# Optimization experiments

Hardware: AMD Instinct MI355X
Metric: run time of the kernel (lower is better)

## Reference

```python
import jax, jax.numpy as jnp
import numpy as np
from jax import lax

IN_CH = 192
CENTER_CH = 192
MID_CH = 192
K = 3
BS, H, W = 8, 64, 64
MASK_NUM = 16


def conv2d(x, w, b, padding=0, groups=1):
    # x: (N,C,H,W), w: (O, I/groups, kh, kw)
    out = lax.conv_general_dilated(
        x, w, window_strides=(1, 1),
        padding=[(padding, padding), (padding, padding)],
        dimension_numbers=('NCHW', 'OIHW', 'NCHW'),
        feature_group_count=groups)
    return out + b[None, :, None, None]


def lrelu(x):
    return jax.nn.leaky_relu(x, negative_slope=0.1)


def setup_inputs() -> dict:
    key = jax.random.key(0)
    ks = jax.random.split(key, 32)
    s = 0.02
    d = {
        'input': jax.random.normal(ks[0], (BS, IN_CH, H, W), jnp.float32),
        'list_center': jax.random.normal(ks[1], (BS, MASK_NUM, CENTER_CH), jnp.float32),
        'batch_mask': jax.random.randint(ks[2], (BS, H, W), 0, MASK_NUM),
        # self.conv: conv1x1(in,mid) -> lrelu -> conv1x1(mid,mid)
        'w0': jax.random.normal(ks[3], (MID_CH, IN_CH, 1, 1)) * s,
        'b0': jnp.zeros((MID_CH,)),
        'w1': jax.random.normal(ks[4], (MID_CH, MID_CH, 1, 1)) * s,
        'b1': jnp.zeros((MID_CH,)),
        # k_sp_gen: conv1x1(mid+center,mid), 3x3(mid,mid), depthwise 3x3(mid -> mid*k^2, groups=mid)
        'ws0': jax.random.normal(ks[5], (MID_CH, MID_CH + CENTER_CH, 1, 1)) * s,
        'bs0': jnp.zeros((MID_CH,)),
        'ws1': jax.random.normal(ks[6], (MID_CH, MID_CH, K, K)) * s,
        'bs1': jnp.zeros((MID_CH,)),
        'ws2': jax.random.normal(ks[7], (MID_CH * K * K, 1, K, K)) * s,
        'bs2': jnp.zeros((MID_CH * K * K,)),
        # k_ch_gen: GAP -> conv1x1 -> lrelu -> conv1x1 -> sigmoid
        'wc0': jax.random.normal(ks[8], (MID_CH, MID_CH, 1, 1)) * s,
        'bc0': jnp.zeros((MID_CH,)),
        'wc1': jax.random.normal(ks[9], (MID_CH, MID_CH, 1, 1)) * s,
        'bc1': jnp.zeros((MID_CH,)),
        # conv_out
        'wo': jax.random.normal(ks[10], (IN_CH, MID_CH, 1, 1)) * s,
        'bo': jnp.zeros((IN_CH,)),
    }
    return d


def mask_expand(list_center, batch_mask):
    # list_center: (bs, mask_num, ch); batch_mask: (bs, h, w) int
    # -> (bs, ch, h, w)
    gathered = jax.vmap(lambda c, m: c[m])(list_center, batch_mask)  # (bs,h,w,ch)
    return jnp.transpose(gathered, (0, 3, 1, 2))


def dynamic_conv(x, k_sp, k):
    # x: (bs, ch, h, w); k_sp: (bs, ch, k^2, h, w)
    bs, ch, h, w = x.shape
    p = (k - 1) // 2
    xp = jnp.pad(x, ((0, 0), (0, 0), (p, p), (p, p)))
    # torch Unfold ordering: kernel index = ki*k + kj, channel-major in view
    patches = jnp.stack([xp[:, :, i:i + h, j:j + w]
                         for i in range(k) for j in range(k)], axis=2)
    return jnp.einsum('bckhw,bckhw->bchw', patches, k_sp)


def reference(input, list_center, batch_mask, w0, b0, w1, b1, ws0, bs0,
              ws1, bs1, ws2, bs2, wc0, bc0, wc1, bc1, wo, bo):
    bs, _, h, w = input.shape
    k = K
    ch = MID_CH
    centers_exp = mask_expand(list_center, batch_mask)  # (bs, center_ch, h, w)
    shortcut = input
    x = conv2d(lrelu(conv2d(input, w0, b0)), w1, b1)  # self.conv
    y = jnp.concatenate([x, centers_exp], axis=1)
    y = lrelu(conv2d(y, ws0, bs0))
    y = lrelu(conv2d(y, ws1, bs1, padding=(k - 1) // 2))
    k_sp = conv2d(y, ws2, bs2, padding=(k - 1) // 2, groups=ch)
    k_sp = k_sp.reshape(bs, ch, k * k, h, w)
    out = dynamic_conv(x, k_sp, k)
    # squeeze-excite channel gate
    g = jnp.mean(out, axis=(2, 3), keepdims=True)
    g = jax.nn.sigmoid(conv2d(lrelu(conv2d(g, wc0, bc0)), wc1, bc1))
    out = g * out
    out = conv2d(out, wo, bo)
    return out + shortcut
```

## Files before the change

### kernel.cpp

```cpp
#include <hip/hip_runtime.h>
#include <hip/hip_bf16.h>

#define CH   192
#define PIX  4096
#define BSZ  8

using f32x4  = __attribute__((ext_vector_type(4))) float;
using short8 = __attribute__((ext_vector_type(8))) short;

__device__ __forceinline__ float bf2f(unsigned short u) {
    union { unsigned u32; float f; } x; x.u32 = ((unsigned)u) << 16; return x.f;
}
__device__ __forceinline__ unsigned short f2bf(float f) {
    union { float f; unsigned u; } x; x.f = f;
    unsigned u = x.u;
    unsigned r = (u + 0x7FFFu + ((u >> 16) & 1u)) >> 16;
    return (unsigned short)r;
}

__device__ __forceinline__ short8 ldsB(const unsigned short* Bsm, int k0, int px) {
    short8 f;
    #pragma unroll
    for (int e = 0; e < 8; ++e) f[e] = (short)Bsm[(k0 + e) * 66 + px];
    return f;
}

__global__ void k_cvt_in(const float* __restrict__ in, unsigned short* __restrict__ out) {
    int i = blockIdx.x * 256 + threadIdx.x;
    float4 v = ((const float4*)in)[i];
    ushort4 o;
    o.x = f2bf(v.x); o.y = f2bf(v.y); o.z = f2bf(v.z); o.w = f2bf(v.w);
    ((ushort4*)out)[i] = o;
}

__global__ void k_prep_w(const float* __restrict__ w0, const float* __restrict__ w1,
                         const float* __restrict__ ws0, const float* __restrict__ wo,
                         const float* __restrict__ ws1,
                         unsigned short* __restrict__ w0f, unsigned short* __restrict__ w1f,
                         unsigned short* __restrict__ ws0xf, unsigned short* __restrict__ wof,
                         unsigned short* __restrict__ wc3f, float* __restrict__ gsum) {
    int i = blockIdx.x * 256 + threadIdx.x;
    if (i < 4*36864) {
        int which = i / 36864, j = i % 36864;
        int kc = j / 6144, r = j % 6144, mf = r / 512, r2 = r % 512;
        int l = r2 >> 3, e = r2 & 7;
        int o = mf*16 + (l & 15), k = kc*32 + ((l >> 4) << 3) + e;
        float v;
        unsigned short* dst;
        if (which == 0)      { v = w0[o*192 + k];  dst = w0f;   }
        else if (which == 1) { v = w1[o*192 + k];  dst = w1f;   }
        else if (which == 2) { v = ws0[o*384 + k]; dst = ws0xf; }
        else                 { v = wo[o*192 + k];  dst = wof;   }
        dst[j] = f2bf(v);
        return;
    }
    i -= 4*36864;
    if (i < 331776) {
        int tk = i / 6144, tap = tk / 6, kc = tk % 6;
        int r = i % 6144, mf = r / 512, r2 = r % 512;
        int l = r2 >> 3, e = r2 & 7;
        int o = mf*16 + (l & 15), c = kc*32 + ((l >> 4) << 3) + e;
        wc3f[i] = f2bf(ws1[(o*192 + c)*9 + tap]);
        return;
    }
    i -= 331776;
    if (i < 1536) gsum[i] = 0.f;
}

__global__ void k_tcent(const float* __restrict__ ws0, const float* __restrict__ lc,
                        float* __restrict__ tc) {
    int m = blockIdx.x, b = blockIdx.y, o = threadIdx.x;
    __shared__ float cbuf[192];
    cbuf[o] = lc[(b*16 + m)*192 + o];
    __syncthreads();
    float a = 0.f;
    const float* wr = ws0 + o*384 + 192;
    for (int c = 0; c < 192; ++c) a += wr[c] * cbuf[c];
    tc[(b*16 + m)*192 + o] = a;
}

__global__ __launch_bounds__(256) void k_fused3(
    const unsigned short* __restrict__ inb,
    const unsigned short* __restrict__ w0f,
    const unsigned short* __restrict__ w1f,
    const unsigned short* __restrict__ ws0xf,
    const float* __restrict__ b0, const float* __restrict__ b1,
    const float* __restrict__ bs0,
    const float* __restrict__ tc, const int* __restrict__ mask,
    unsigned short* __restrict__ xg, unsigned short* __restrict__ y0g)
{
    const int b = blockIdx.y, n0 = blockIdx.x * 64;
    __shared__ unsigned short Bsm[192*66];
    __shared__ unsigned short Csm[192*66];
    const int tid = threadIdx.x, lane = tid & 63, wv = tid >> 6;
    const int li = lane & 15, kq = lane >> 4;

    {
        const unsigned short* src = inb + (size_t)b*192*PIX + n0;
        #pragma unroll
        for (int j = 0; j < 6; ++j) {
            int q = tid + 256*j, k = q >> 3, g = q & 7;
            uint4 v = *(const uint4*)(src + (size_t)k*PIX + g*8);
            unsigned* d = (unsigned*)(Bsm + k*66 + g*8);
            const unsigned* s = (const unsigned*)&v;
            d[0]=s[0]; d[1]=s[1]; d[2]=s[2]; d[3]=s[3];
        }
    }
    __syncthreads();

    f32x4 acc[3][4];

    #pragma unroll
    for (int m = 0; m < 3; ++m)
        #pragma unroll
        for (int n = 0; n < 4; ++n) acc[m][n] = {0.f,0.f,0.f,0.f};
    for (int kc = 0; kc < 6; ++kc) {
        short8 a[3];
        #pragma unroll
        for (int m = 0; m < 3; ++m)
            a[m] = *(const short8*)(w0f + ((kc*12 + wv*3 + m)*64 + lane)*8);
        #pragma unroll
        for (int n = 0; n < 4; ++n) {
            short8 fb = ldsB(Bsm, kc*32 + kq*8, n*16 + li);
            #pragma unroll
            for (int m = 0; m < 3; ++m)
                acc[m][n] = __builtin_amdgcn_mfma_f32_16x16x32_bf16(a[m], fb, acc[m][n], 0,0,0);
        }
    }
    #pragma unroll
    for (int m = 0; m < 3; ++m) {
        int o0 = (wv*3 + m)*16 + kq*4;
        #pragma unroll
        for (int n = 0; n < 4; ++n) {
            int px = n*16 + li;
            #pragma unroll
            for (int r = 0; r < 4; ++r) {
                float v = acc[m][n][r] + b0[o0 + r];
                v = v > 0.f ? v : 0.1f*v;
                Csm[(o0 + r)*66 + px] = f2bf(v);
            }
        }
    }
    __syncthreads();

    #pragma unroll
    for (int m = 0; m < 3; ++m)
        #pragma unroll
        for (int n = 0; n < 4; ++n) acc[m][n] = {0.f,0.f,0.f,0.f};
    for (int kc = 0; kc < 6; ++kc) {
        short8 a[3];
        #pragma unroll
        for (int m = 0; m < 3; ++m)
            a[m] = *(const short8*)(w1f + ((kc*12 + wv*3 + m)*64 + lane)*8);
        #pragma unroll
        for (int n = 0; n < 4; ++n) {
            short8 fb = ldsB(Csm, kc*32 + kq*8, n*16 + li);
            #pragma unroll
            for (int m = 0; m < 3; ++m)
                acc[m][n] = __builtin_amdgcn_mfma_f32_16x16x32_bf16(a[m], fb, acc[m][n], 0,0,0);
        }
    }
    #pragma unroll
    for (int m = 0; m < 3; ++m) {
        int o0 = (wv*3 + m)*16 + kq*4;
        #pragma unroll
        for (int n = 0; n < 4; ++n) {
            int px = n*16 + li;
            #pragma unroll
            for (int r = 0; r < 4; ++r) {
                float v = acc[m][n][r] + b1[o0 + r];
                unsigned short h = f2bf(v);
                Bsm[(o0 + r)*66 + px] = h;
                xg[((size_t)b*192 + o0 + r)*PIX + n0 + px] = h;
            }
        }
    }
    __syncthreads();

    #pragma unroll
    for (int m = 0; m < 3; ++m)
        #pragma unroll
        for (int n = 0; n < 4; ++n) acc[m][n] = {0.f,0.f,0.f,0.f};
    for (int kc = 0; kc < 6; ++kc) {
        short8 a[3];
        #pragma unroll
        for (int m = 0; m < 3; ++m)
            a[m] = *(const short8*)(ws0xf + ((kc*12 + wv*3 + m)*64 + lane)*8);
        #pragma unroll
        for (int n = 0; n < 4; ++n) {
            short8 fb = ldsB(Bsm, kc*32 + kq*8, n*16 + li);
            #pragma unroll
            for (int m = 0; m < 3; ++m)
                acc[m][n] = __builtin_amdgcn_mfma_f32_16x16x32_bf16(a[m], fb, acc[m][n], 0,0,0);
        }
    }
    int mi_[4];
    #pragma unroll
    for (int n = 0; n < 4; ++n) mi_[n] = mask[b*PIX + n0 + n*16 + li];
    #pragma unroll
    for (int m = 0; m < 3; ++m) {
        int o0 = (wv*3 + m)*16 + kq*4;
        #pragma unroll
        for (int n = 0; n < 4; ++n) {
            int px = n*16 + li;
            const float* tcb = tc + (b*16 + mi_[n])*192;
            #pragma unroll
            for (int r = 0; r < 4; ++r) {
                float v = acc[m][n][r] + bs0[o0 + r] + tcb[o0 + r];
                v = v > 0.f ? v : 0.1f*v;
                y0g[((size_t)b*192 + o0 + r)*PIX + n0 + px] = f2bf(v);
            }
        }
    }
}

__global__ __launch_bounds__(256) void k_conv3n(
    const unsigned short* __restrict__ wc3f,
    const unsigned short* __restrict__ y0,
    const float* __restrict__ bias,
    unsigned short* __restrict__ y1)
{
    const int b = blockIdx.y, h = blockIdx.x;
    __shared__ unsigned short Bs[3*32*66];
    const int tid = threadIdx.x, lane = tid & 63, wv = tid >> 6;
    const int li = lane & 15, kq = lane >> 4;

    f32x4 acc[3][4];
    #pragma unroll
    for (int m = 0; m < 3; ++m)
        #pragma unroll
        for (int n = 0; n < 4; ++n) acc[m][n] = {0.f,0.f,0.f,0.f};

    if (tid < 96) Bs[tid*66] = 0;
    else if (tid < 192) Bs[(tid-96)*66 + 65] = 0;

    for (int kc = 0; kc < 6; ++kc) {
        #pragma unroll
        for (int j = 0; j < 3; ++j) {
            int q = tid*3 + j;
            int dr = q >> 8, k = (q >> 3) & 31, w8 = (q & 7)*8;
            int hh = h + dr - 1;
            uint4 v = {0u,0u,0u,0u};
            if (hh >= 0 && hh < 64)
                v = *(const uint4*)(y0 + ((size_t)b*192 + kc*32 + k)*PIX + hh*64 + w8);
            const unsigned short* pv = (const unsigned short*)&v;
            unsigned short* dst = Bs + (dr*32 + k)*66 + 1 + w8;
            #pragma unroll
            for (int e = 0; e < 8; ++e) dst[e] = pv[e];
        }
        __syncthreads();

        #pragma unroll
        for (int tap = 0; tap < 9; ++tap) {
            const int dr = tap / 3, dc1 = tap % 3;
            short8 a[3];
            #pragma unroll
            for (int m = 0; m < 3; ++m)
                a[m] = *(const short8*)(wc3f + (((tap*6 + kc)*12 + wv*3 + m)*64 + lane)*8);
            #pragma unroll
            for (int n = 0; n < 4; ++n) {
                short8 fb = ldsB(Bs + dr*32*66, kq*8, n*16 + li + dc1);
                #pragma unroll
                for (int m = 0; m < 3; ++m)
                    acc[m][n] = __builtin_amdgcn_mfma_f32_16x16x32_bf16(a[m], fb, acc[m][n], 0,0,0);
            }
        }
        __syncthreads();
    }

    #pragma unroll
    for (int m = 0; m < 3; ++m) {
        int o0 = (wv*3 + m)*16 + kq*4;
        #pragma unroll
        for (int n = 0; n < 4; ++n) {
            int px = h*64 + n*16 + li;
            #pragma unroll
            for (int r = 0; r < 4; ++r) {
                float v = acc[m][n][r] + bias[o0 + r];
                v = v > 0.f ? v : 0.1f*v;
                y1[((size_t)b*192 + o0 + r)*PIX + px] = f2bf(v);
            }
        }
    }
}

__global__ __launch_bounds__(256) void k_dwdyn2(
    const unsigned short* __restrict__ Y1,
    const unsigned short* __restrict__ X,
    const float* __restrict__ ws2,
    const float* __restrict__ bs2,
    unsigned short* __restrict__ OP,
    float* __restrict__ gsum)
{
    const int c = blockIdx.x, b = blockIdx.y;
    __shared__ unsigned short ysm[4096];
    __shared__ unsigned short xsm[4096];
    __shared__ float wsm[81], bsm9[9], red[4];
    const int tid = threadIdx.x;
    const size_t cb = ((size_t)b*192 + c) * PIX;
    #pragma unroll
    for (int j = 0; j < 2; ++j) {
        int i = tid + 256*j;
        *(uint4*)(ysm + i*8) = *(const uint4*)(Y1 + cb + i*8);
        *(uint4*)(xsm + i*8) = *(const uint4*)(X  + cb + i*8);
    }
    if (tid < 81) wsm[tid] = ws2[c*81 + tid];
    else if (tid < 90) bsm9[tid-81] = bs2[c*9 + tid - 81];
    __syncthreads();

    float gacc = 0.f;
    for (int i = 0; i < 16; ++i) {
        int px = tid + 256*i, hh = px >> 6, ww = px & 63;
        float ksp[9];
        #pragma unroll
        for (int j = 0; j < 9; ++j) ksp[j] = bsm9[j];
        #pragma unroll
        for (int tap = 0; tap < 9; ++tap) {
            int h2 = hh + tap/3 - 1, w2 = ww + tap%3 - 1;
            float yv = ((unsigned)h2 < 64u && (unsigned)w2 < 64u)
                       ? bf2f(ysm[h2*64 + w2]) : 0.f;
            #pragma unroll
            for (int j = 0; j < 9; ++j) ksp[j] += yv * wsm[j*9 + tap];
        }
        float out = 0.f;
        #pragma unroll
        for (int j = 0; j < 9; ++j) {
            int h2 = hh + j/3 - 1, w2 = ww + j%3 - 1;
            float xv = ((unsigned)h2 < 64u && (unsigned)w2 < 64u)
                       ? bf2f(xsm[h2*64 + w2]) : 0.f;
            out += xv * ksp[j];
        }
        OP[cb + px] = f2bf(out);
        gacc += out;
    }
    #pragma unroll
    for (int off = 32; off > 0; off >>= 1) gacc += __shfl_down(gacc, off);
    if ((tid & 63) == 0) red[tid >> 6] = gacc;
    __syncthreads();
    if (tid == 0) gsum[b*192 + c] = red[0] + red[1] + red[2] + red[3];
}

__global__ void k_gate(const float* __restrict__ gsum,
                       const float* __restrict__ wc0, const float* __restrict__ bc0,
                       const float* __restrict__ wc1, const float* __restrict__ bc1,
                       float* __restrict__ gvec)
{
    const int b = blockIdx.x, t = threadIdx.x;
    __shared__ float mean[192], s1[192];
    mean[t] = gsum[b*192 + t] * (1.f/4096.f);
    __syncthreads();
    float a = bc0[t];
    const float* w = wc0 + t*192;
    for (int i = 0; i < 192; ++i) a += w[i] * mean[i];
    s1[t] = a > 0.f ? a : 0.1f * a;
    __syncthreads();
    float a2 = bc1[t];
    const float* w2 = wc1 + t*192;
    for (int i = 0; i < 192; ++i) a2 += w2[i] * s1[i];
    gvec[b*192 + t] = 1.f / (1.f + __expf(-a2));
}

__global__ __launch_bounds__(256) void k_gemmo(
    const unsigned short* __restrict__ wof,
    const unsigned short* __restrict__ op,
    const float* __restrict__ bo,
    const float* __restrict__ gvec,
    const float* __restrict__ resid,
    float* __restrict__ out)
{
    const int b = blockIdx.y, n0 = blockIdx.x * 64;
    __shared__ unsigned short Bsm[192*66];
    const int tid = threadIdx.x, lane = tid & 63, wv = tid >> 6;
    const int li = lane & 15, kq = lane >> 4;

    {
        const unsigned short* src = op + (size_t)b*192*PIX + n0;
        #pragma unroll
        for (int j = 0; j < 6; ++j) {
            int q = tid + 256*j, k = q >> 3, g = q & 7;
            uint4 v = *(const uint4*)(src + (size_t)k*PIX + g*8);
            float gs = gvec[b*192 + k];
            unsigned short* pv = (unsigned short*)&v;
            #pragma unroll
            for (int e = 0; e < 8; ++e) pv[e] = f2bf(bf2f(pv[e]) * gs);
            unsigned* d = (unsigned*)(Bsm + k*66 + g*8);
            const unsigned* s = (const unsigned*)&v;
            d[0]=s[0]; d[1]=s[1]; d[2]=s[2]; d[3]=s[3];
        }
    }
    __syncthreads();

    f32x4 acc[3][4];
    #pragma unroll
    for (int m = 0; m < 3; ++m)
        #pragma unroll
        for (int n = 0; n < 4; ++n) acc[m][n] = {0.f,0.f,0.f,0.f};
    for (int kc = 0; kc < 6; ++kc) {
        short8 a[3];
        #pragma unroll
        for (int m = 0; m < 3; ++m)
            a[m] = *(const short8*)(wof + ((kc*12 + wv*3 + m)*64 + lane)*8);
        #pragma unroll
        for (int n = 0; n < 4; ++n) {
            short8 fb = ldsB(Bsm, kc*32 + kq*8, n*16 + li);
            #pragma unroll
            for (int m = 0; m < 3; ++m)
                acc[m][n] = __builtin_amdgcn_mfma_f32_16x16x32_bf16(a[m], fb, acc[m][n], 0,0,0);
        }
    }
    #pragma unroll
    for (int m = 0; m < 3; ++m) {
        int o0 = (wv*3 + m)*16 + kq*4;
        #pragma unroll
        for (int n = 0; n < 4; ++n) {
            int px = n*16 + li;
            #pragma unroll
            for (int r = 0; r < 4; ++r) {
                size_t idx = ((size_t)b*192 + o0 + r)*PIX + n0 + px;
                out[idx] = acc[m][n][r] + bo[o0 + r] + resid[idx];
            }
        }
    }
}

extern "C" void kernel_launch(void* const* d_in, const int* in_sizes, int n_in,
                              void* d_out, int out_size, void* d_ws, size_t ws_size,
                              hipStream_t stream)
{
    const float* input = (const float*)d_in[0];
    const float* lc    = (const float*)d_in[1];
    const int*   mask  = (const int*)d_in[2];
    const float* w0  = (const float*)d_in[3];
    const float* b0  = (const float*)d_in[4];
    const float* w1  = (const float*)d_in[5];
    const float* b1  = (const float*)d_in[6];
    const float* ws0 = (const float*)d_in[7];
    const float* bs0 = (const float*)d_in[8];
    const float* ws1 = (const float*)d_in[9];
    const float* bs1 = (const float*)d_in[10];
    const float* ws2 = (const float*)d_in[11];
    const float* bs2 = (const float*)d_in[12];
    const float* wc0 = (const float*)d_in[13];
    const float* bc0 = (const float*)d_in[14];
    const float* wc1 = (const float*)d_in[15];
    const float* bc1 = (const float*)d_in[16];
    const float* wo  = (const float*)d_in[17];
    const float* bo  = (const float*)d_in[18];

    char* ws = (char*)d_ws;
    size_t off = 0;
    auto alloc = [&](size_t bytes) {
        void* p = ws + off; off = (off + bytes + 255) & ~(size_t)255; return p;
    };
    const size_t act_b = (size_t)BSZ * CH * PIX * 2;
    unsigned short* in_bf = (unsigned short*)alloc(act_b);
    unsigned short* x_bf  = (unsigned short*)alloc(act_b);
    unsigned short* y0_bf = (unsigned short*)alloc(act_b);
    unsigned short* y1_bf = (unsigned short*)alloc(act_b);
    unsigned short* op_bf = (unsigned short*)alloc(act_b);
    unsigned short* w0f   = (unsigned short*)alloc(36864*2);
    unsigned short* w1f   = (unsigned short*)alloc(36864*2);
    unsigned short* ws0xf = (unsigned short*)alloc(36864*2);
    unsigned short* wof   = (unsigned short*)alloc(36864*2);
    unsigned short* wc3f  = (unsigned short*)alloc(331776*2);
    float* tc   = (float*)alloc(8*16*192*4);
    float* gsum = (float*)alloc(1536*4);
    float* gvec = (float*)alloc(1536*4);

    k_cvt_in<<<6144, 256, 0, stream>>>(input, in_bf);
    k_prep_w<<<1878, 256, 0, stream>>>(w0, w1, ws0, wo, ws1, w0f, w1f, ws0xf, wof, wc3f, gsum);
    k_tcent<<<dim3(16, 8), 192, 0, stream>>>(ws0, lc, tc);

    dim3 gg(64, 8);
    k_fused3<<<gg, 256, 0, stream>>>(in_bf, w0f, w1f, ws0xf, b0, b1, bs0, tc, mask, x_bf, y0_bf);
    k_conv3n<<<gg, 256, 0, stream>>>(wc3f, y0_bf, bs1, y1_bf);
    k_dwdyn2<<<dim3(192, 8), 256, 0, stream>>>(y1_bf, x_bf, ws2, bs2, op_bf, gsum);
    k_gate<<<8, 192, 0, stream>>>(gsum, wc0, bc0, wc1, bc1, gvec);
    k_gemmo<<<gg, 256, 0, stream>>>(wof, op_bf, bo, gvec, input, (float*)d_out);
}
```

Measured before the change: 246.9 us.

## Fuse input bf16 cast into first GEMM and use pixel-major y0 for 3x3 conv

Drops the separate fp32-to-bf16 input conversion kernel: the fused 1x1 GEMM kernel now reads fp32 input and converts it while staging into LDS. The y0 intermediate is written channel-contiguous (pixel-major), going through an LDS transpose, so the 3x3 conv kernel can load 16-byte B fragments straight from LDS instead of gathering 8 scalar shorts. The 3x3 conv moves to 512 threads with the pixel tile split across wave pairs. An extra barrier and a padded Csm stride are added so the new transpose can reuse Csm safely, at the cost of more shared memory.

```diff
diff --git a/kernel.cpp b/kernel.cpp
--- a/kernel.cpp
+++ b/kernel.cpp
@@ -18,19 +18,11 @@
     return (unsigned short)r;
 }
 
-__device__ __forceinline__ short8 ldsB(const unsigned short* Bsm, int k0, int px) {
+__device__ __forceinline__ short8 ldsBs(const unsigned short* B, int ST, int k0, int px) {
     short8 f;
     #pragma unroll
-    for (int e = 0; e < 8; ++e) f[e] = (short)Bsm[(k0 + e) * 66 + px];
+    for (int e = 0; e < 8; ++e) f[e] = (short)B[(k0 + e) * ST + px];
     return f;
-}
-
-__global__ void k_cvt_in(const float* __restrict__ in, unsigned short* __restrict__ out) {
-    int i = blockIdx.x * 256 + threadIdx.x;
-    float4 v = ((const float4*)in)[i];
-    ushort4 o;
-    o.x = f2bf(v.x); o.y = f2bf(v.y); o.z = f2bf(v.z); o.w = f2bf(v.w);
-    ((ushort4*)out)[i] = o;
 }
 
 __global__ void k_prep_w(const float* __restrict__ w0, const float* __restrict__ w1,
@@ -80,30 +72,34 @@
 }
 
 __global__ __launch_bounds__(256) void k_fused3(
-    const unsigned short* __restrict__ inb,
+    const float* __restrict__ input,
     const unsigned short* __restrict__ w0f,
     const unsigned short* __restrict__ w1f,
     const unsigned short* __restrict__ ws0xf,
     const float* __restrict__ b0, const float* __restrict__ b1,
     const float* __restrict__ bs0,
     const float* __restrict__ tc, const int* __restrict__ mask,
-    unsigned short* __restrict__ xg, unsigned short* __restrict__ y0g)
+    unsigned short* __restrict__ xg, unsigned short* __restrict__ y0t)
 {
     const int b = blockIdx.y, n0 = blockIdx.x * 64;
     __shared__ unsigned short Bsm[192*66];
-    __shared__ unsigned short Csm[192*66];
+    __shared__ unsigned short Csm[192*67];
     const int tid = threadIdx.x, lane = tid & 63, wv = tid >> 6;
     const int li = lane & 15, kq = lane >> 4;
 
     {
-        const unsigned short* src = inb + (size_t)b*192*PIX + n0;
+        const float* src = input + (size_t)b*192*PIX + n0;
         #pragma unroll
         for (int j = 0; j < 6; ++j) {
-            int q = tid + 256*j, k = q >> 3, g = q & 7;
-            uint4 v = *(const uint4*)(src + (size_t)k*PIX + g*8);
-            unsigned* d = (unsigned*)(Bsm + k*66 + g*8);
-            const unsigned* s = (const unsigned*)&v;
-            d[0]=s[0]; d[1]=s[1]; d[2]=s[2]; d[3]=s[3];
+            int q = tid + 256*j, k = q >> 3, g = (q & 7)*8;
+            float4 v0 = *(const float4*)(src + (size_t)k*PIX + g);
+            float4 v1 = *(const float4*)(src + (size_t)k*PIX + g + 4);
+            unsigned d0 = f2bf(v0.x) | ((unsigned)f2bf(v0.y) << 16);
+            unsigned d1 = f2bf(v0.z) | ((unsigned)f2bf(v0.w) << 16);
+            unsigned d2 = f2bf(v1.x) | ((unsigned)f2bf(v1.y) << 16);
+            unsigned d3 = f2bf(v1.z) | ((unsigned)f2bf(v1.w) << 16);
+            unsigned* d = (unsigned*)(Bsm + k*66 + g);
+            d[0]=d0; d[1]=d1; d[2]=d2; d[3]=d3;
         }
     }
     __syncthreads();
@@ -121,7 +117,7 @@
             a[m] = *(const short8*)(w0f + ((kc*12 + wv*3 + m)*64 + lane)*8);
         #pragma unroll
         for (int n = 0; n < 4; ++n) {
-            short8 fb = ldsB(Bsm, kc*32 + kq*8, n*16 + li);
+            short8 fb = ldsBs(Bsm, 66, kc*32 + kq*8, n*16 + li);
             #pragma unroll
             for (int m = 0; m < 3; ++m)
                 acc[m][n] = __builtin_amdgcn_mfma_f32_16x16x32_bf16(a[m], fb, acc[m][n], 0,0,0);
@@ -137,7 +133,7 @@
             for (int r = 0; r < 4; ++r) {
                 float v = acc[m][n][r] + b0[o0 + r];
                 v = v > 0.f ? v : 0.1f*v;
-                Csm[(o0 + r)*66 + px] = f2bf(v);
+                Csm[(o0 + r)*67 + px] = f2bf(v);
             }
         }
     }
@@ -154,12 +150,13 @@
             a[m] = *(const short8*)(w1f + ((kc*12 + wv*3 + m)*64 + lane)*8);
         #pragma unroll
         for (int n = 0; n < 4; ++n) {
-            short8 fb = ldsB(Csm, kc*32 + kq*8, n*16 + li);
+            short8 fb = ldsBs(Csm, 67, kc*32 + kq*8, n*16 + li);
             #pragma unroll
             for (int m = 0; m < 3; ++m)
                 acc[m][n] = __builtin_amdgcn_mfma_f32_16x16x32_bf16(a[m], fb, acc[m][n], 0,0,0);
         }
     }
+    __syncthreads();
     #pragma unroll
     for (int m = 0; m < 3; ++m) {
         int o0 = (wv*3 + m)*16 + kq*4;
@@ -188,7 +185,7 @@
             a[m] = *(const short8*)(ws0xf + ((kc*12 + wv*3 + m)*64 + lane)*8);
         #pragma unroll
         for (int n = 0; n < 4; ++n) {
-            short8 fb = ldsB(Bsm, kc*32 + kq*8, n*16 + li);
+            short8 fb = ldsBs(Bsm, 66, kc*32 + kq*8, n*16 + li);
             #pragma unroll
             for (int m = 0; m < 3; ++m)
                 acc[m][n] = __builtin_amdgcn_mfma_f32_16x16x32_bf16(a[m], fb, acc[m][n], 0,0,0);
@@ -204,49 +201,54 @@
         for (int n = 0; n < 4; ++n) {
             int px = n*16 + li;
             const float* tcb = tc + (b*16 + mi_[n])*192;
+            ushort4 w;
+            unsigned short* wp = (unsigned short*)&w;
             #pragma unroll
             for (int r = 0; r < 4; ++r) {
                 float v = acc[m][n][r] + bs0[o0 + r] + tcb[o0 + r];
                 v = v > 0.f ? v : 0.1f*v;
-                y0g[((size_t)b*192 + o0 + r)*PIX + n0 + px] = f2bf(v);
-            }
-        }
-    }
-}
-
-__global__ __launch_bounds__(256) void k_conv3n(
+                wp[r] = f2bf(v);
+            }
+            *(ushort4*)(Csm + px*200 + o0) = w;
+        }
+    }
+    __syncthreads();
+    #pragma unroll
+    for (int j = 0; j < 6; ++j) {
+        int u = tid + 256*j;
+        int px = u / 24, chunk = u % 24;
+        uint4 v = *(const uint4*)(Csm + px*200 + chunk*8);
+        *(uint4*)(y0t + ((size_t)(b*4096 + n0 + px))*192 + chunk*8) = v;
+    }
+}
+
+__global__ __launch_bounds__(512) void k_conv3t(
     const unsigned short* __restrict__ wc3f,
-    const unsigned short* __restrict__ y0,
+    const unsigned short* __restrict__ y0t,
     const float* __restrict__ bias,
     unsigned short* __restrict__ y1)
 {
     const int b = blockIdx.y, h = blockIdx.x;
-    __shared__ unsigned short Bs[3*32*66];
+    __shared__ unsigned short Bs[3*66*40];
     const int tid = threadIdx.x, lane = tid & 63, wv = tid >> 6;
     const int li = lane & 15, kq = lane >> 4;
-
-    f32x4 acc[3][4];
+    const int mw = wv >> 1, nh = wv & 1;
+
+    f32x4 acc[3][2];
     #pragma unroll
     for (int m = 0; m < 3; ++m)
         #pragma unroll
-        for (int n = 0; n < 4; ++n) acc[m][n] = {0.f,0.f,0.f,0.f};
-
-    if (tid < 96) Bs[tid*66] = 0;
-    else if (tid < 192) Bs[(tid-96)*66 + 65] = 0;
+        for (int nn = 0; nn < 2; ++nn) acc[m][nn] = {0.f,0.f,0.f,0.f};
 
     for (int kc = 0; kc < 6; ++kc) {
-        #pragma unroll
-        for (int j = 0; j < 3; ++j) {
-            int q = tid*3 + j;
-            int dr = q >> 8, k = (q >> 3) & 31, w8 = (q & 7)*8;
-            int hh = h + dr - 1;
+        for (int u = tid; u < 792; u += 512) {
+            int row = u >> 2, chunk = u & 3;
+            int dr = row / 66, pxl = row % 66;
+            int hh = h + dr - 1, pxg = pxl - 1;
             uint4 v = {0u,0u,0u,0u};
-            if (hh >= 0 && hh < 64)
-                v = *(const uint4*)(y0 + ((size_t)b*192 + kc*32 + k)*PIX + hh*64 + w8);
-            const unsigned short* pv = (const unsigned short*)&v;
-            unsigned short* dst = Bs + (dr*32 + k)*66 + 1 + w8;
-            #pragma unroll
-            for (int e = 0; e < 8; ++e) dst[e] = pv[e];
+            if ((unsigned)hh < 64u && (unsigned)pxg < 64u)
+                v = *(const uint4*)(y0t + ((size_t)(b*4096 + hh*64 + pxg))*192 + kc*32 + chunk*8);
+            *(uint4*)((char*)Bs + row*80 + chunk*16) = v;
         }
         __syncthreads();
 
@@ -256,13 +258,14 @@
             short8 a[3];
             #pragma unroll
             for (int m = 0; m < 3; ++m)
-                a[m] = *(const short8*)(wc3f + (((tap*6 + kc)*12 + wv*3 + m)*64 + lane)*8);
-            #pragma unroll
-            for (int n = 0; n < 4; ++n) {
-                short8 fb = ldsB(Bs + dr*32*66, kq*8, n*16 + li + dc1);
+                a[m] = *(const short8*)(wc3f + (((tap*6 + kc)*12 + mw*3 + m)*64 + lane)*8);
+            #pragma unroll
+            for (int nn = 0; nn < 2; ++nn) {
+                int pxi = nh*32 + nn*16 + li + dc1;
+                short8 fb = *(const short8*)((const char*)Bs + (dr*66 + pxi)*80 + kq*16);
                 #pragma unroll
                 for (int m = 0; m < 3; ++m)
-                    acc[m][n] = __builtin_amdgcn_mfma_f32_16x16x32_bf16(a[m], fb, acc[m][n], 0,0,0);
+                    acc[m][nn] = __builtin_amdgcn_mfma_f32_16x16x32_bf16(a[m], fb, acc[m][nn], 0,0,0);
             }
         }
         __syncthreads();
@@ -270,13 +273,13 @@
 
     #pragma unroll
     for (int m = 0; m < 3; ++m) {
-        int o0 = (wv*3 + m)*16 + kq*4;
-        #pragma unroll
-        for (int n = 0; n < 4; ++n) {
-            int px = h*64 + n*16 + li;
+        int o0 = (mw*3 + m)*16 + kq*4;
+        #pragma unroll
+        for (int nn = 0; nn < 2; ++nn) {
+            int px = h*64 + nh*32 + nn*16 + li;
             #pragma unroll
             for (int r = 0; r < 4; ++r) {
-                float v = acc[m][n][r] + bias[o0 + r];
+                float v = acc[m][nn][r] + bias[o0 + r];
                 v = v > 0.f ? v : 0.1f*v;
                 y1[((size_t)b*192 + o0 + r)*PIX + px] = f2bf(v);
             }
@@ -377,13 +380,13 @@
         const unsigned short* src = op + (size_t)b*192*PIX + n0;
         #pragma unroll
         for (int j = 0; j < 6; ++j) {
-            int q = tid + 256*j, k = q >> 3, g = q & 7;
-            uint4 v = *(const uint4*)(src + (size_t)k*PIX + g*8);
+            int q = tid + 256*j, k = q >> 3, g = (q & 7) * 8;
+            uint4 v = *(const uint4*)(src + (size_t)k*PIX + g);
             float gs = gvec[b*192 + k];
             unsigned short* pv = (unsigned short*)&v;
             #pragma unroll
             for (int e = 0; e < 8; ++e) pv[e] = f2bf(bf2f(pv[e]) * gs);
-            unsigned* d = (unsigned*)(Bsm + k*66 + g*8);
+            unsigned* d = (unsigned*)(Bsm + k*66 + g);
             const unsigned* s = (const unsigned*)&v;
             d[0]=s[0]; d[1]=s[1]; d[2]=s[2]; d[3]=s[3];
         }
@@ -402,7 +405,7 @@
             a[m] = *(const short8*)(wof + ((kc*12 + wv*3 + m)*64 + lane)*8);
         #pragma unroll
         for (int n = 0; n < 4; ++n) {
-            short8 fb = ldsB(Bsm, kc*32 + kq*8, n*16 + li);
+            short8 fb = ldsBs(Bsm, 66, kc*32 + kq*8, n*16 + li);
             #pragma unroll
             for (int m = 0; m < 3; ++m)
                 acc[m][n] = __builtin_amdgcn_mfma_f32_16x16x32_bf16(a[m], fb, acc[m][n], 0,0,0);
@@ -453,9 +456,8 @@
         void* p = ws + off; off = (off + bytes + 255) & ~(size_t)255; return p;
     };
     const size_t act_b = (size_t)BSZ * CH * PIX * 2;
-    unsigned short* in_bf = (unsigned short*)alloc(act_b);
     unsigned short* x_bf  = (unsigned short*)alloc(act_b);
-    unsigned short* y0_bf = (unsigned short*)alloc(act_b);
+    unsigned short* y0t   = (unsigned short*)alloc(act_b);
     unsigned short* y1_bf = (unsigned short*)alloc(act_b);
     unsigned short* op_bf = (unsigned short*)alloc(act_b);
     unsigned short* w0f   = (unsigned short*)alloc(36864*2);
@@ -467,13 +469,12 @@
     float* gsum = (float*)alloc(1536*4);
     float* gvec = (float*)alloc(1536*4);
 
-    k_cvt_in<<<6144, 256, 0, stream>>>(input, in_bf);
     k_prep_w<<<1878, 256, 0, stream>>>(w0, w1, ws0, wo, ws1, w0f, w1f, ws0xf, wof, wc3f, gsum);
     k_tcent<<<dim3(16, 8), 192, 0, stream>>>(ws0, lc, tc);
 
     dim3 gg(64, 8);
-    k_fused3<<<gg, 256, 0, stream>>>(in_bf, w0f, w1f, ws0xf, b0, b1, bs0, tc, mask, x_bf, y0_bf);
-    k_conv3n<<<gg, 256, 0, stream>>>(wc3f, y0_bf, bs1, y1_bf);
+    k_fused3<<<gg, 256, 0, stream>>>(input, w0f, w1f, ws0xf, b0, b1, bs0, tc, mask, x_bf, y0t);
+    k_conv3t<<<gg, 512, 0, stream>>>(wc3f, y0t, bs1, y1_bf);
     k_dwdyn2<<<dim3(192, 8), 256, 0, stream>>>(y1_bf, x_bf, ws2, bs2, op_bf, gsum);
     k_gate<<<8, 192, 0, stream>>>(gsum, wc0, bc0, wc1, bc1, gvec);
     k_gemmo<<<gg, 256, 0, stream>>>(wof, op_bf, bo, gvec, input, (float*)d_out);
```

Result: faster. 232.2 us (-6.0%).
